# Performance work log

Hardware: AMD Instinct MI355X
Metric: run time of the kernel (lower is better)

## Reference

```python
import jax, jax.numpy as jnp
import numpy as np

HIDDEN = 768
MLP_HIDDEN = 3072
HEADS = 12
HEAD_DIM = HIDDEN // HEADS

def setup_inputs() -> dict:
    key = jax.random.key(0)
    ks = jax.random.split(key, 12)
    s = 0.02
    return {
        "x": jax.random.normal(ks[0], (16, 1024, HIDDEN), dtype=jnp.float32),
        "ln1_g": jnp.ones((HIDDEN,), jnp.float32),
        "ln1_b": jnp.zeros((HIDDEN,), jnp.float32),
        "wq": jax.random.normal(ks[1], (HIDDEN, HIDDEN), jnp.float32) * s,
        "wk": jax.random.normal(ks[2], (HIDDEN, HIDDEN), jnp.float32) * s,
        "wv": jax.random.normal(ks[3], (HIDDEN, HIDDEN), jnp.float32) * s,
        "wo": jax.random.normal(ks[4], (HIDDEN, HIDDEN), jnp.float32) * s,
        "bo": jnp.zeros((HIDDEN,), jnp.float32),
        "ln2_g": jnp.ones((HIDDEN,), jnp.float32),
        "ln2_b": jnp.zeros((HIDDEN,), jnp.float32),
        "w1": jax.random.normal(ks[5], (HIDDEN, MLP_HIDDEN), jnp.float32) * s,
        "b1": jnp.zeros((MLP_HIDDEN,), jnp.float32),
        "w2": jax.random.normal(ks[6], (MLP_HIDDEN, HIDDEN), jnp.float32) * s,
        "b2": jnp.zeros((HIDDEN,), jnp.float32),
    }

def _layernorm(x, g, b, eps=1e-5):
    mu = jnp.mean(x, axis=-1, keepdims=True)
    var = jnp.mean(jnp.square(x - mu), axis=-1, keepdims=True)
    return (x - mu) * jax.lax.rsqrt(var + eps) * g + b

def reference(x, ln1_g, ln1_b, wq, wk, wv, wo, bo, ln2_g, ln2_b, w1, b1, w2, b2):
    b, n, _ = x.shape
    h, d = HEADS, HEAD_DIM
    scale = d ** -0.5
    # Attention branch
    xn = _layernorm(x, ln1_g, ln1_b)
    q = (xn @ wq.T).reshape(b, n, h, d).transpose(0, 2, 1, 3)  # bhnd
    k = (xn @ wk.T).reshape(b, n, h, d).transpose(0, 2, 1, 3)
    v = (xn @ wv.T).reshape(b, n, h, d).transpose(0, 2, 1, 3)
    score = jax.nn.softmax(jnp.einsum('bhif,bhjf->bhij', q, k) * scale, axis=-1)
    attn = jnp.einsum('bhij,bhjf->bihf', score, v).reshape(b, n, h * d)
    x = attn @ wo.T + bo + x
    # MLP branch
    xn = _layernorm(x, ln2_g, ln2_b)
    hdn = jax.nn.gelu(xn @ w1 + b1, approximate=False)
    x = hdn @ w2 + b2 + x
    return x
```

## Files before the change

kernel.cpp:

```cpp
#include <hip/hip_runtime.h>
#include <hip/hip_bf16.h>

#define HIDDEN 768
#define MLPH   3072
#define HEADS  12
#define HD     64
#define SEQ    1024
#define BATCH  16
#define MTOT   (BATCH*SEQ)

typedef __attribute__((ext_vector_type(8))) short  short8;
typedef __attribute__((ext_vector_type(4))) short  short4x;
typedef __attribute__((ext_vector_type(8))) __bf16 bf16x8;
typedef __attribute__((ext_vector_type(4))) float  floatx4;

#define CL2 0.18033688011112042f

__device__ inline short f2bf(float f) {
  __hip_bfloat16 h = __float2bfloat16(f);
  return *reinterpret_cast<short*>(&h);
}

__device__ inline floatx4 mfma_bf16(short8 a, short8 b, floatx4 c) {
  return __builtin_amdgcn_mfma_f32_16x16x32_bf16(
      __builtin_bit_cast(bf16x8, a), __builtin_bit_cast(bf16x8, b), c, 0, 0, 0);
}

__device__ inline void gl_lds16(const short* g, short* l) {
  __builtin_amdgcn_global_load_lds(
      (const __attribute__((address_space(1))) unsigned int*)g,
      (__attribute__((address_space(3))) unsigned int*)l, 16, 0, 0);
}

__device__ inline float gelu_f(float x) {
  float z = 0.7978845608028654f * (x + 0.044715f * x * x * x);
  float e = __builtin_amdgcn_exp2f(z * 2.8853900817779268f);
  float t = 1.0f - 2.0f * __builtin_amdgcn_rcpf(e + 1.0f);
  return 0.5f * x * (1.0f + t);
}

__global__ __launch_bounds__(256) void conv_weights(
    const float* __restrict__ wq, const float* __restrict__ wk,
    const float* __restrict__ wv, const float* __restrict__ wo,
    const float* __restrict__ w1, const float* __restrict__ w2,
    short* __restrict__ wqkvb, short* __restrict__ wob,
    short* __restrict__ w1t,   short* __restrict__ w2t)
{
  int i = blockIdx.x * 256 + threadIdx.x;
  const int HH = HIDDEN * HIDDEN;
  if (i < HH) {
    wqkvb[i]        = f2bf(wq[i]);
    wqkvb[HH + i]   = f2bf(wk[i]);
    wqkvb[2*HH + i] = f2bf(wv[i]);
    wob[i]          = f2bf(wo[i]);
  }
  if (i < HIDDEN * MLPH) {
    int n = i / HIDDEN, k = i % HIDDEN;
    w1t[i] = f2bf(w1[(size_t)k * MLPH + n]);
    int n2 = i / MLPH, k2 = i % MLPH;
    w2t[i] = f2bf(w2[(size_t)k2 * HIDDEN + n2]);
  }
}

__global__ __launch_bounds__(256) void ln_kernel(
    const float* __restrict__ x, const float* __restrict__ g,
    const float* __restrict__ b, short* __restrict__ out)
{
  int row = blockIdx.x;
  const float* xr = x + (size_t)row * HIDDEN;
  int t = threadIdx.x;
  float v0 = xr[t], v1 = xr[t + 256], v2 = xr[t + 512];
  float s  = v0 + v1 + v2;
  float s2 = v0*v0 + v1*v1 + v2*v2;
  for (int off = 32; off > 0; off >>= 1) {
    s  += __shfl_down(s, off);
    s2 += __shfl_down(s2, off);
  }
  __shared__ float red[8];
  __shared__ float stats[2];
  int wave = t >> 6;
  if ((t & 63) == 0) { red[wave] = s; red[4 + wave] = s2; }
  __syncthreads();
  if (t == 0) {
    float S  = red[0] + red[1] + red[2] + red[3];
    float S2 = red[4] + red[5] + red[6] + red[7];
    float mu  = S * (1.0f / HIDDEN);
    float var = S2 * (1.0f / HIDDEN) - mu * mu;
    stats[0] = mu;
    stats[1] = rsqrtf(var + 1e-5f);
  }
  __syncthreads();
  float mu = stats[0], rs = stats[1];
  short* orow = out + (size_t)row * HIDDEN;
  orow[t]       = f2bf((v0 - mu) * rs * g[t]       + b[t]);
  orow[t + 256] = f2bf((v1 - mu) * rs * g[t + 256] + b[t + 256]);
  orow[t + 512] = f2bf((v2 - mu) * rs * g[t + 512] + b[t + 512]);
}

template<int OUTMODE , bool BIAS, bool GELU_E, bool RES,
         bool SCALEQ = false>
__global__ __launch_bounds__(512, 2) void gemm_bt2(
    const short* __restrict__ A, const short* __restrict__ B,
    const float* __restrict__ bias, const float* __restrict__ res,
    void* __restrict__ out, int M, int N, int K)
{
  __shared__ alignas(16) short As[2][2][8192];
  __shared__ alignas(16) short Bs[2][2][8192];

  int tid = threadIdx.x;
  int lane = tid & 63, wave = tid >> 6;
  int wr = wave >> 2, wc = wave & 3;
  int quad = lane >> 4, lc = lane & 15;

  int nbx = gridDim.x;
  int nwg = nbx * gridDim.y;
  int orig = blockIdx.y * nbx + blockIdx.x;
  int q8 = nwg >> 3, r8 = nwg & 7;
  int xcd = orig & 7, sub = orig >> 3;
  int wg = (xcd < r8 ? xcd * (q8 + 1) : r8 * (q8 + 1) + (xcd - r8) * q8) + sub;
  int m0 = (wg / nbx) * 256;
  int n0 = (wg % nbx) * 256;

  int srow = tid >> 2;
  int skb  = (tid & 3) ^ ((srow >> 1) & 3);
  const short* ga = A + (size_t)(m0 + srow) * K + skb * 8;
  const short* gb = B + (size_t)(n0 + srow) * K + skb * 8;
  const size_t rowskip = (size_t)128 * K;
  int lb0 = wave * 512;

#define STAGE_R(MAT, gp, sl, ks, kt) {                         \
    const short* _g = (gp) + (size_t)(kt) * 64 + (ks) * 32;    \
    gl_lds16(_g,           &MAT[sl][ks][lb0]);                 \
    gl_lds16(_g + rowskip, &MAT[sl][ks][4096 + lb0]);          \
  }

  floatx4 acc[8][4];
#pragma unroll
  for (int i = 0; i < 8; ++i)
#pragma unroll
    for (int j = 0; j < 4; ++j) acc[i][j] = floatx4{0.f, 0.f, 0.f, 0.f};

  int apos = (quad ^ ((lc >> 1) & 3)) * 8;
#define RD(buf, r) (*(const short8*)&(buf)[(r) * 32 + apos])
#define MM4x4(IOFF)                                                     \
    _Pragma("unroll")                                                   \
    for (int i = 0; i < 4; ++i)                                         \
      _Pragma("unroll")                                                 \
      for (int j = 0; j < 4; ++j)                                       \
        acc[i + IOFF][j] = mfma_bf16(aF[i], bF[j], acc[i + IOFF][j]);

  int NK = K >> 6;

  STAGE_R(As, ga, 0, 0, 0); STAGE_R(Bs, gb, 0, 0, 0);
  STAGE_R(As, ga, 0, 1, 0); STAGE_R(Bs, gb, 0, 1, 0);

  for (int kt = 0; kt < NK; ++kt) {
    const int sl = kt & 1;
    const short (*as_)[8192] = As[sl];
    const short (*bs_)[8192] = Bs[sl];
    const int s2 = sl ^ 1;
    const bool st = (kt + 1 < NK);
    short8 aF[4], bF[4];

    asm volatile("s_waitcnt vmcnt(2)" ::: "memory");
    __builtin_amdgcn_s_barrier();
    asm volatile("" ::: "memory");
#pragma unroll
    for (int i = 0; i < 4; ++i) aF[i] = RD(as_[0], wr * 128 + i * 16 + lc);
#pragma unroll
    for (int j = 0; j < 4; ++j) bF[j] = RD(bs_[0], wc * 64 + j * 16 + lc);
    if (st) STAGE_R(Bs, gb, s2, 1, kt + 1);
    asm volatile("s_waitcnt lgkmcnt(0)" ::: "memory");
    __builtin_amdgcn_sched_barrier(0);
    __builtin_amdgcn_s_setprio(1);
    MM4x4(0);
    __builtin_amdgcn_s_setprio(0);

    __builtin_amdgcn_s_barrier();
    asm volatile("" ::: "memory");
#pragma unroll
    for (int i = 0; i < 4; ++i) aF[i] = RD(as_[0], wr * 128 + (i + 4) * 16 + lc);
    if (st) STAGE_R(Bs, gb, s2, 0, kt + 1);
    asm volatile("s_waitcnt lgkmcnt(0)" ::: "memory");
    __builtin_amdgcn_sched_barrier(0);
    __builtin_amdgcn_s_setprio(1);
    MM4x4(4);
    __builtin_amdgcn_s_setprio(0);

    if (st) asm volatile("s_waitcnt vmcnt(4)" ::: "memory");
    else    asm volatile("s_waitcnt vmcnt(0)" ::: "memory");
    __builtin_amdgcn_s_barrier();
    asm volatile("" ::: "memory");
#pragma unroll
    for (int i = 0; i < 4; ++i) aF[i] = RD(as_[1], wr * 128 + i * 16 + lc);
#pragma unroll
    for (int j = 0; j < 4; ++j) bF[j] = RD(bs_[1], wc * 64 + j * 16 + lc);
    if (st) STAGE_R(As, ga, s2, 0, kt + 1);
    asm volatile("s_waitcnt lgkmcnt(0)" ::: "memory");
    __builtin_amdgcn_sched_barrier(0);
    __builtin_amdgcn_s_setprio(1);
    MM4x4(0);
    __builtin_amdgcn_s_setprio(0);

    __builtin_amdgcn_s_barrier();
    asm volatile("" ::: "memory");
#pragma unroll
    for (int i = 0; i < 4; ++i) aF[i] = RD(as_[1], wr * 128 + (i + 4) * 16 + lc);
    if (st) STAGE_R(As, ga, s2, 1, kt + 1);
    asm volatile("s_waitcnt lgkmcnt(0)" ::: "memory");
    __builtin_amdgcn_sched_barrier(0);
    __builtin_amdgcn_s_setprio(1);
    MM4x4(4);
    __builtin_amdgcn_s_setprio(0);
  }
#undef STAGE_R
#undef RD
#undef MM4x4

#pragma unroll
  for (int i = 0; i < 8; ++i)
#pragma unroll
    for (int j = 0; j < 4; ++j)
#pragma unroll
      for (int r = 0; r < 4; ++r) {
        int row = m0 + wr * 128 + i * 16 + quad * 4 + r;
        int col = n0 + wc * 64 + j * 16 + lc;
        float v = acc[i][j][r];
        if (BIAS)   v += bias[col];
        if (GELU_E) v = gelu_f(v);
        if (RES)    v += res[(size_t)row * N + col];
        if (SCALEQ && col < HIDDEN) v *= CL2;
        if (OUTMODE == 1) ((short*)out)[(size_t)row * N + col] = f2bf(v);
        else              ((float*)out)[(size_t)row * N + col] = v;
      }
}

__global__ __launch_bounds__(256) void vtrans_kernel(
    const short* __restrict__ qkv, short* __restrict__ vtg)
{
  int kt = blockIdx.x, h = blockIdx.y, b = blockIdx.z;
  int t = threadIdx.x;
  __shared__ short Vl[64][72];
  const short* vb = qkv + (size_t)(b * SEQ + kt * 64) * 2304 + 1536 + h * 64;
  int row = t >> 2, seg = t & 3;
  short8 r0 = *(const short8*)(vb + (size_t)row * 2304 + seg * 16);
  short8 r1 = *(const short8*)(vb + (size_t)row * 2304 + seg * 16 + 8);
  *(short8*)&Vl[row][seg * 16]     = r0;
  *(short8*)&Vl[row][seg * 16 + 8] = r1;
  __syncthreads();
  int ks = t >> 7, d = (t & 127) >> 1, hb = t & 1;
  short8 w0;
#pragma unroll
  for (int u = 0; u < 8; ++u) {
    int blk = hb * 2 + (u >> 3), j = u & 7;
    int ksrc = ks * 32 + (blk ^ ((d >> 1) & 3)) * 8 + j;
    w0[u] = Vl[ksrc][d];
  }
  short8 w1;
#pragma unroll
  for (int u = 8; u < 16; ++u) {
    int blk = hb * 2 + (u >> 3), j = u & 7;
    int ksrc = ks * 32 + (blk ^ ((d >> 1) & 3)) * 8 + j;
    w1[u - 8] = Vl[ksrc][d];
  }
  short* o = vtg + ((size_t)((b * HEADS + h) * 16 + kt)) * 4096 + t * 16;
  *(short8*)o       = w0;
  *(short8*)(o + 8) = w1;
}

__global__ __launch_bounds__(512) void attn_kernel(
    const short* __restrict__ qkv, const short* __restrict__ vtg,
    short* __restrict__ out)
{
  int qt = blockIdx.x;
  int h  = blockIdx.y;
  int b  = blockIdx.z;
  int tid = threadIdx.x, lane = tid & 63, wave = tid >> 6;
  int quad = lane >> 4, lc = lane & 15;

  __shared__ alignas(16) short Qs[2 * 128 * 32];
  __shared__ alignas(16) short Ks[2 * 64 * 32];
  __shared__ alignas(16) short Vs[2 * 64 * 32];
  __shared__ alignas(16) short Ps[8][16 * 72];

  const int LDQ = 3 * HIDDEN;
  const short* qb = qkv + (size_t)(b * SEQ) * LDQ + h * HD;
  const short* kb = qb + HIDDEN;
  const short* vt = vtg + (size_t)((b * HEADS + h) * 16) * 4096;

  {
    int row = tid >> 2, blk = tid & 3;
    int kblk = blk ^ ((row >> 1) & 3);
#pragma unroll
    for (int t = 0; t < 2; ++t) {
      const short* g = qb + (size_t)(qt * 128 + row) * LDQ + t * 32 + kblk * 8;
      gl_lds16(g, &Qs[t * 4096 + wave * 512]);
    }
  }
  __syncthreads();

  int pos = quad ^ ((lc >> 1) & 3);
  short8 aq[2];
#pragma unroll
  for (int ks = 0; ks < 2; ++ks)
    aq[ks] = *(const short8*)&Qs[ks * 4096 + (wave * 16 + lc) * 32 + pos * 8];

  floatx4 oacc[4];
#pragma unroll
  for (int n2 = 0; n2 < 4; ++n2) oacc[n2] = floatx4{0.f, 0.f, 0.f, 0.f};
  float lsum = 0.f;

  int srow = (tid >> 2) & 63;
  int sks  = tid >> 8;
  int skb  = (tid & 3) ^ ((srow >> 1) & 3);
  const short* kg0 = kb + (size_t)srow * LDQ + sks * 32 + skb * 8;
  const short* vg0 = vt + tid * 8;
  short* pw = &Ps[wave][0];

  for (int kt = 0; kt < 16; ++kt) {
    gl_lds16(kg0 + (size_t)(kt * 64) * LDQ, &Ks[wave * 512]);
    gl_lds16(vg0 + kt * 4096, &Vs[wave * 512]);
    __syncthreads();

    floatx4 sacc[4];
#pragma unroll
    for (int m2 = 0; m2 < 4; ++m2) sacc[m2] = floatx4{0.f, 0.f, 0.f, 0.f};
#pragma unroll
    for (int ks = 0; ks < 2; ++ks) {
#pragma unroll
      for (int m2 = 0; m2 < 4; ++m2) {
        short8 ak = *(const short8*)&Ks[ks * 2048 + (m2 * 16 + lc) * 32 + pos * 8];
        sacc[m2] = mfma_bf16(ak, aq[ks], sacc[m2]);
      }
    }

#pragma unroll
    for (int m2 = 0; m2 < 4; ++m2) {
      float p0 = exp2f(sacc[m2][0]);
      float p1 = exp2f(sacc[m2][1]);
      float p2 = exp2f(sacc[m2][2]);
      float p3 = exp2f(sacc[m2][3]);
      lsum += (p0 + p1) + (p2 + p3);
      short4x pk;
      pk[0] = f2bf(p0); pk[1] = f2bf(p1); pk[2] = f2bf(p2); pk[3] = f2bf(p3);
      *(short4x*)&pw[lc * 72 + m2 * 16 + quad * 4] = pk;
    }
    asm volatile("s_waitcnt lgkmcnt(0)" ::: "memory");
    __builtin_amdgcn_sched_barrier(0);

#pragma unroll
    for (int ks = 0; ks < 2; ++ks) {
      short8 ap = *(const short8*)&pw[lc * 72 + (ks * 4 + quad) * 8];
#pragma unroll
      for (int n2 = 0; n2 < 4; ++n2) {
        short8 bv = *(const short8*)&Vs[ks * 2048 + (n2 * 16 + lc) * 32 + pos * 8];
        oacc[n2] = mfma_bf16(ap, bv, oacc[n2]);
      }
    }
    __syncthreads();
  }

  float rs = lsum;
  rs += __shfl_xor(rs, 16);
  rs += __shfl_xor(rs, 32);
#pragma unroll
  for (int r = 0; r < 4; ++r) {
    float inv = 1.0f / __shfl(rs, quad * 4 + r);
    int row = b * SEQ + qt * 128 + wave * 16 + quad * 4 + r;
#pragma unroll
    for (int n2 = 0; n2 < 4; ++n2) {
      int col = h * HD + n2 * 16 + lc;
      out[(size_t)row * HIDDEN + col] = f2bf(oacc[n2][r] * inv);
    }
  }
}

extern "C" void kernel_launch(void* const* d_in, const int* in_sizes, int n_in,
                              void* d_out, int out_size, void* d_ws, size_t ws_size,
                              hipStream_t stream) {
  const float* x    = (const float*)d_in[0];
  const float* ln1g = (const float*)d_in[1];
  const float* ln1b = (const float*)d_in[2];
  const float* wq   = (const float*)d_in[3];
  const float* wk   = (const float*)d_in[4];
  const float* wv   = (const float*)d_in[5];
  const float* wo   = (const float*)d_in[6];
  const float* bo   = (const float*)d_in[7];
  const float* ln2g = (const float*)d_in[8];
  const float* ln2b = (const float*)d_in[9];
  const float* w1   = (const float*)d_in[10];
  const float* b1   = (const float*)d_in[11];
  const float* w2   = (const float*)d_in[12];
  const float* b2   = (const float*)d_in[13];

  auto rup = [](size_t b) { return (b + 255) & ~(size_t)255; };
  const size_t wbytes = rup((size_t)3 * HIDDEN * HIDDEN * 2) +
                        rup((size_t)HIDDEN * HIDDEN * 2) +
                        rup((size_t)MLPH * HIDDEN * 2) +
                        rup((size_t)HIDDEN * MLPH * 2);

  int R = SEQ;
  const int cands[4] = {16384, 8192, 4096, 2048};
  for (int i = 0; i < 4; ++i) {
    size_t need = wbytes + rup((size_t)cands[i] * 1536) + rup((size_t)cands[i] * 6144)
                         + rup((size_t)cands[i] * 1536);
    if (need <= ws_size) { R = cands[i]; break; }
  }

  char* ws = (char*)d_ws;
  size_t off = 0;
  auto alloc = [&](size_t bytes) {
    char* p = ws + off;
    off += (bytes + 255) & ~(size_t)255;
    return p;
  };
  short* wqkvb = (short*)alloc((size_t)3 * HIDDEN * HIDDEN * 2);
  short* wob   = (short*)alloc((size_t)HIDDEN * HIDDEN * 2);
  short* w1t   = (short*)alloc((size_t)MLPH * HIDDEN * 2);
  short* w2t   = (short*)alloc((size_t)HIDDEN * MLPH * 2);
  short* slotA = (short*)alloc((size_t)R * 1536);
  short* bigR  = (short*)alloc((size_t)R * 6144);
  short* vtg   = (short*)alloc((size_t)R * 1536);

  conv_weights<<<(HIDDEN * MLPH + 255) / 256, 256, 0, stream>>>(
      wq, wk, wv, wo, w1, w2, wqkvb, wob, w1t, w2t);

  const int nch = MTOT / R;
  for (int c = 0; c < nch; ++c) {
    const float* xc  = x + (size_t)c * R * HIDDEN;
    float*       x2c = (float*)d_out + (size_t)c * R * HIDDEN;

    ln_kernel<<<R, 256, 0, stream>>>(xc, ln1g, ln1b, slotA);
    gemm_bt2<1, false, false, false, true>
        <<<dim3((3 * HIDDEN) / 256, R / 256), 512, 0, stream>>>(
        slotA, wqkvb, nullptr, nullptr, bigR, R, 3 * HIDDEN, HIDDEN);
    vtrans_kernel<<<dim3(16, HEADS, R / SEQ), 256, 0, stream>>>(bigR, vtg);
    attn_kernel<<<dim3(SEQ / 128, HEADS, R / SEQ), 512, 0, stream>>>(
        bigR, vtg, slotA);
    gemm_bt2<0, true, false, true>
        <<<dim3(HIDDEN / 256, R / 256), 512, 0, stream>>>(
        slotA, wob, bo, xc, x2c, R, HIDDEN, HIDDEN);
    ln_kernel<<<R, 256, 0, stream>>>(x2c, ln2g, ln2b, slotA);
    gemm_bt2<1, true, true, false>
        <<<dim3(MLPH / 256, R / 256), 512, 0, stream>>>(
        slotA, w1t, b1, nullptr, bigR, R, MLPH, HIDDEN);
    gemm_bt2<0, true, false, true>
        <<<dim3(HIDDEN / 256, R / 256), 512, 0, stream>>>(
        bigR, w2t, b2, x2c, x2c, R, HIDDEN, MLPH);
  }
}
```

Measured before the change: 565.9 us.

## Fuse V transpose into QKV GEMM epilogue and tile weight transposes

The QKV GEMM epilogue now writes the V columns straight into the swizzled, transposed per-head layout the attention kernel reads, so the separate vtrans kernel and its extra pass over V are gone. The w1/w2 fp32-to-bf16 transposes move to an LDS-tiled transpose kernel, replacing the strided uncoalesced reads in conv_weights. The risk is that the V epilogue stores are scattered 2-byte writes, which may coalesce poorly inside the GEMM.

New measurement: 568.1 us. About the same (+0.4%).

```diff
diff --git a/kernel.cpp b/kernel.cpp
--- a/kernel.cpp
+++ b/kernel.cpp
@@ -42,9 +42,7 @@
 __global__ __launch_bounds__(256) void conv_weights(
     const float* __restrict__ wq, const float* __restrict__ wk,
     const float* __restrict__ wv, const float* __restrict__ wo,
-    const float* __restrict__ w1, const float* __restrict__ w2,
-    short* __restrict__ wqkvb, short* __restrict__ wob,
-    short* __restrict__ w1t,   short* __restrict__ w2t)
+    short* __restrict__ wqkvb, short* __restrict__ wob)
 {
   int i = blockIdx.x * 256 + threadIdx.x;
   const int HH = HIDDEN * HIDDEN;
@@ -54,12 +52,21 @@
     wqkvb[2*HH + i] = f2bf(wv[i]);
     wob[i]          = f2bf(wo[i]);
   }
-  if (i < HIDDEN * MLPH) {
-    int n = i / HIDDEN, k = i % HIDDEN;
-    w1t[i] = f2bf(w1[(size_t)k * MLPH + n]);
-    int n2 = i / MLPH, k2 = i % MLPH;
-    w2t[i] = f2bf(w2[(size_t)k2 * HIDDEN + n2]);
-  }
+}
+
+__global__ __launch_bounds__(256) void wtrans_kernel(
+    const float* __restrict__ in, short* __restrict__ out, int RK, int CN)
+{
+  __shared__ float T[64][65];
+  int n0 = blockIdx.x * 64, k0 = blockIdx.y * 64;
+  int tx = threadIdx.x & 63, ty = threadIdx.x >> 6;
+#pragma unroll
+  for (int r = ty; r < 64; r += 4)
+    T[r][tx] = in[(size_t)(k0 + r) * CN + n0 + tx];
+  __syncthreads();
+#pragma unroll
+  for (int r = ty; r < 64; r += 4)
+    out[(size_t)(n0 + r) * RK + k0 + tx] = f2bf(T[tx][r]);
 }
 
 __global__ __launch_bounds__(256) void ln_kernel(
@@ -98,11 +105,11 @@
 }
 
 template<int OUTMODE , bool BIAS, bool GELU_E, bool RES,
-         bool SCALEQ = false>
+         bool SCALEQ = false, bool VSPLIT = false>
 __global__ __launch_bounds__(512, 2) void gemm_bt2(
     const short* __restrict__ A, const short* __restrict__ B,
     const float* __restrict__ bias, const float* __restrict__ res,
-    void* __restrict__ out, int M, int N, int K)
+    void* __restrict__ out, short* __restrict__ vout, int M, int N, int K)
 {
   __shared__ alignas(16) short As[2][2][8192];
   __shared__ alignas(16) short Bs[2][2][8192];
@@ -230,42 +237,20 @@
         if (GELU_E) v = gelu_f(v);
         if (RES)    v += res[(size_t)row * N + col];
         if (SCALEQ && col < HIDDEN) v *= CL2;
-        if (OUTMODE == 1) ((short*)out)[(size_t)row * N + col] = f2bf(v);
-        else              ((float*)out)[(size_t)row * N + col] = v;
+        if (VSPLIT && col >= 2 * HIDDEN) {
+          int b_ = row >> 10, rr = row & 1023, kt_ = rr >> 6, k_ = rr & 63;
+          int ks_ = k_ >> 5, kk = k_ & 31;
+          int hd = col - 2 * HIDDEN, h_ = hd >> 6, d_ = hd & 63;
+          size_t idx = ((size_t)((b_ * HEADS + h_) * 16 + kt_)) * 4096
+                     + ks_ * 2048 + d_ * 32
+                     + (((kk >> 3) ^ ((d_ >> 1) & 3)) << 3) + (kk & 7);
+          vout[idx] = f2bf(v);
+        } else if (OUTMODE == 1) {
+          ((short*)out)[(size_t)row * N + col] = f2bf(v);
+        } else {
+          ((float*)out)[(size_t)row * N + col] = v;
+        }
       }
-}
-
-__global__ __launch_bounds__(256) void vtrans_kernel(
-    const short* __restrict__ qkv, short* __restrict__ vtg)
-{
-  int kt = blockIdx.x, h = blockIdx.y, b = blockIdx.z;
-  int t = threadIdx.x;
-  __shared__ short Vl[64][72];
-  const short* vb = qkv + (size_t)(b * SEQ + kt * 64) * 2304 + 1536 + h * 64;
-  int row = t >> 2, seg = t & 3;
-  short8 r0 = *(const short8*)(vb + (size_t)row * 2304 + seg * 16);
-  short8 r1 = *(const short8*)(vb + (size_t)row * 2304 + seg * 16 + 8);
-  *(short8*)&Vl[row][seg * 16]     = r0;
-  *(short8*)&Vl[row][seg * 16 + 8] = r1;
-  __syncthreads();
-  int ks = t >> 7, d = (t & 127) >> 1, hb = t & 1;
-  short8 w0;
-#pragma unroll
-  for (int u = 0; u < 8; ++u) {
-    int blk = hb * 2 + (u >> 3), j = u & 7;
-    int ksrc = ks * 32 + (blk ^ ((d >> 1) & 3)) * 8 + j;
-    w0[u] = Vl[ksrc][d];
-  }
-  short8 w1;
-#pragma unroll
-  for (int u = 8; u < 16; ++u) {
-    int blk = hb * 2 + (u >> 3), j = u & 7;
-    int ksrc = ks * 32 + (blk ^ ((d >> 1) & 3)) * 8 + j;
-    w1[u - 8] = Vl[ksrc][d];
-  }
-  short* o = vtg + ((size_t)((b * HEADS + h) * 16 + kt)) * 4096 + t * 16;
-  *(short8*)o       = w0;
-  *(short8*)(o + 8) = w1;
 }
 
 __global__ __launch_bounds__(512) void attn_kernel(
@@ -422,8 +407,12 @@
   short* bigR  = (short*)alloc((size_t)R * 6144);
   short* vtg   = (short*)alloc((size_t)R * 1536);
 
-  conv_weights<<<(HIDDEN * MLPH + 255) / 256, 256, 0, stream>>>(
-      wq, wk, wv, wo, w1, w2, wqkvb, wob, w1t, w2t);
+  conv_weights<<<(HIDDEN * HIDDEN + 255) / 256, 256, 0, stream>>>(
+      wq, wk, wv, wo, wqkvb, wob);
+  wtrans_kernel<<<dim3(MLPH / 64, HIDDEN / 64), 256, 0, stream>>>(
+      w1, w1t, HIDDEN, MLPH);
+  wtrans_kernel<<<dim3(HIDDEN / 64, MLPH / 64), 256, 0, stream>>>(
+      w2, w2t, MLPH, HIDDEN);
 
   const int nch = MTOT / R;
   for (int c = 0; c < nch; ++c) {
@@ -431,21 +420,20 @@
     float*       x2c = (float*)d_out + (size_t)c * R * HIDDEN;
 
     ln_kernel<<<R, 256, 0, stream>>>(xc, ln1g, ln1b, slotA);
-    gemm_bt2<1, false, false, false, true>
+    gemm_bt2<1, false, false, false, true, true>
         <<<dim3((3 * HIDDEN) / 256, R / 256), 512, 0, stream>>>(
-        slotA, wqkvb, nullptr, nullptr, bigR, R, 3 * HIDDEN, HIDDEN);
-    vtrans_kernel<<<dim3(16, HEADS, R / SEQ), 256, 0, stream>>>(bigR, vtg);
+        slotA, wqkvb, nullptr, nullptr, bigR, vtg, R, 3 * HIDDEN, HIDDEN);
     attn_kernel<<<dim3(SEQ / 128, HEADS, R / SEQ), 512, 0, stream>>>(
         bigR, vtg, slotA);
     gemm_bt2<0, true, false, true>
         <<<dim3(HIDDEN / 256, R / 256), 512, 0, stream>>>(
-        slotA, wob, bo, xc, x2c, R, HIDDEN, HIDDEN);
+        slotA, wob, bo, xc, x2c, nullptr, R, HIDDEN, HIDDEN);
     ln_kernel<<<R, 256, 0, stream>>>(x2c, ln2g, ln2b, slotA);
     gemm_bt2<1, true, true, false>
         <<<dim3(MLPH / 256, R / 256), 512, 0, stream>>>(
-        slotA, w1t, b1, nullptr, bigR, R, MLPH, HIDDEN);
+        slotA, w1t, b1, nullptr, bigR, nullptr, R, MLPH, HIDDEN);
     gemm_bt2<0, true, false, true>
         <<<dim3(HIDDEN / 256, R / 256), 512, 0, stream>>>(
-        bigR, w2t, b2, x2c, x2c, R, HIDDEN, MLPH);
-  }
-}
+        bigR, w2t, b2, x2c, x2c, nullptr, R, HIDDEN, MLPH);
+  }
+}
```
